# Kernel optimization log

Measured on AMD Instinct MI355X. Metric: run time of the kernel, lower is better.

The kernel has to match this reference:

```python
import jax, jax.numpy as jnp
import numpy as np

IN_F = 1024
OUT_F = 1024
GRID = 8
TOKENS = 8192


def setup_inputs() -> dict:
    key = jax.random.key(0)
    k_x, k_w, k_b, k_s = jax.random.split(key, 4)
    x = jax.random.normal(k_x, (TOKENS, IN_F), dtype=jnp.float32)
    # kaiming_uniform_(nonlinearity='linear'): bound = sqrt(3/fan_in)
    bound_w = float(np.sqrt(3.0 / IN_F))
    W = jax.random.uniform(k_w, (OUT_F, IN_F), minval=-bound_w, maxval=bound_w, dtype=jnp.float32)
    # nn.Linear default bias init: U(-1/sqrt(fan_in), 1/sqrt(fan_in))
    bound_b = float(1.0 / np.sqrt(IN_F))
    b = jax.random.uniform(k_b, (OUT_F,), minval=-bound_b, maxval=bound_b, dtype=jnp.float32)
    spline_weight = jax.random.uniform(k_s, (OUT_F, IN_F, GRID), minval=-0.1, maxval=0.1, dtype=jnp.float32)
    grid = jnp.linspace(-3.0, 3.0, GRID, dtype=jnp.float32)
    return {"x": x, "W": W, "b": b, "spline_weight": spline_weight, "grid": grid}


def reference(x, W, b, spline_weight, grid):
    grid_size = spline_weight.shape[-1]
    # base path: Linear(silu(x))
    base = jnp.einsum('ti,oi->to', jax.nn.silu(x), W) + b
    # RBF basis: [tokens, in_features, grid_size]
    denom = 2.0 / (grid_size - 1) + 1e-05
    basis = jnp.exp(-(((x[..., None] - grid) / denom) ** 2))
    spline = jnp.einsum('tig,oig->to', basis, spline_weight)
    return base + spline
```

## Files before the change

### kernel.cpp

```cpp
#include <hip/hip_runtime.h>
#include <hip/hip_bf16.h>

#define IN_F   1024
#define OUT_F  1024
#define GRID_N 8
#define TOKENS 8192
#define KTOT   9216
#define KHALF  4608
#define NTILE  72

typedef __attribute__((ext_vector_type(8))) short  bf16x8;
typedef __attribute__((ext_vector_type(4))) float  f32x4;

template<int M> struct ModeT { static constexpr int value = M; };

__device__ __forceinline__ unsigned int f2bf(float f) {
    union { float f; unsigned int u; } v; v.f = f;
    unsigned int r = v.u + 0x7fffu + ((v.u >> 16) & 1u);
    return r >> 16;
}

__global__ __launch_bounds__(256)
void prep_a_kernel(const float* __restrict__ x, const float* __restrict__ grid,
                   unsigned short* __restrict__ A)
{
    int idx = blockIdx.x * blockDim.x + threadIdx.x;
    int t = idx >> 10;
    int i = idx & 1023;
    float xv = x[idx];
    float sil = xv / (1.0f + __expf(-xv));
    A[(size_t)t * KTOT + i] = (unsigned short)f2bf(sil);

    const float invd = 1.0f / (2.0f / 7.0f + 1e-5f);
    unsigned int h[8];
    #pragma unroll
    for (int g = 0; g < 8; ++g) {
        float d = (xv - grid[g]) * invd;
        h[g] = f2bf(__expf(-d * d));
    }
    uint4 pk;
    pk.x = h[0] | (h[1] << 16);
    pk.y = h[2] | (h[3] << 16);
    pk.z = h[4] | (h[5] << 16);
    pk.w = h[6] | (h[7] << 16);
    *reinterpret_cast<uint4*>(&A[(size_t)t * KTOT + IN_F + (size_t)i * 8]) = pk;
}

__global__ __launch_bounds__(256)
void prep_b_kernel(const float* __restrict__ W, const float* __restrict__ spl,
                   unsigned short* __restrict__ B)
{
    int idx = blockIdx.x * blockDim.x + threadIdx.x;
    int o  = idx / (KTOT / 8);
    int c8 = idx - o * (KTOT / 8);
    const float* src = (c8 < IN_F / 8)
        ? (W   + (size_t)o * IN_F            + (size_t)c8 * 8)
        : (spl + (size_t)o * (IN_F * GRID_N) + (size_t)(c8 - IN_F / 8) * 8);
    const float4* s4 = reinterpret_cast<const float4*>(src);
    float4 lo = s4[0], hi = s4[1];
    uint4 pk;
    pk.x = f2bf(lo.x) | (f2bf(lo.y) << 16);
    pk.y = f2bf(lo.z) | (f2bf(lo.w) << 16);
    pk.z = f2bf(hi.x) | (f2bf(hi.y) << 16);
    pk.w = f2bf(hi.z) | (f2bf(hi.w) << 16);
    *reinterpret_cast<uint4*>(&B[(size_t)o * KTOT + (size_t)c8 * 8]) = pk;
}

#define GLOAD(src, dst) __builtin_amdgcn_global_load_lds( \
    (const __attribute__((address_space(1))) void*)(src),  \
    (__attribute__((address_space(3))) void*)(dst), 16, 0, 0)
#define SBAR()  __builtin_amdgcn_s_barrier()
#define SCH0()  __builtin_amdgcn_sched_barrier(0)
#define LGKM0() asm volatile("s_waitcnt lgkmcnt(0)" ::: "memory")
#define VMCNT_(n) asm volatile("s_waitcnt vmcnt(" #n ")" ::: "memory")

__global__ __launch_bounds__(512, 2)
void gemm_kan2(const unsigned short* __restrict__ A,
               const unsigned short* __restrict__ B,
               float* __restrict__ P, int rows)
{
    __shared__ char lds[131072];

    const int bid  = blockIdx.x;
    const int sk   = bid & 1;
    const int bn   = (bid >> 1) & 3;
    const int bm   = bid >> 3;
    const int tid  = threadIdx.x;
    const int wave = tid >> 6, lane = tid & 63;
    const int wr   = wave >> 2, wc = wave & 3;
    const int fr   = lane & 15, kg = lane >> 4;
    const int sw   = fr & 7;
    const int koff[2] = { (kg ^ sw) * 16, ((4 | kg) ^ sw) * 16 };
    const int k0 = sk * KHALF;

    const int trow = tid >> 3;
    const int ksrc = ((tid & 7) ^ (trow & 7)) * 8;
    const unsigned short* gA = A + (size_t)(bm * 256 + trow) * KTOT + k0 + ksrc;
    const unsigned short* gB = B + (size_t)(bn * 256 + trow) * KTOT + k0 + ksrc;
    const size_t R64 = (size_t)64 * KTOT;

    f32x4 acc[8][4];
    const f32x4 zero = {0.f, 0.f, 0.f, 0.f};
    #pragma unroll
    for (int m = 0; m < 8; ++m)
        #pragma unroll
        for (int n = 0; n < 4; ++n) acc[m][n] = zero;

    {
        char* d = lds + tid * 16;
        GLOAD(gA,           d);            GLOAD(gA + R64,     d + 8192);
        GLOAD(gB,           d + 32768);    GLOAD(gB + R64,     d + 40960);
        GLOAD(gB + 2 * R64, d + 49152);    GLOAD(gB + 3 * R64, d + 57344);
        GLOAD(gA + 2 * R64, d + 16384);    GLOAD(gA + 3 * R64, d + 24576);
        gA += 64; gB += 64;
        d += 65536;
        GLOAD(gA,           d);            GLOAD(gA + R64,     d + 8192);
        GLOAD(gB,           d + 32768);    GLOAD(gB + R64,     d + 40960);
        GLOAD(gB + 2 * R64, d + 49152);    GLOAD(gB + 3 * R64, d + 57344);
        GLOAD(gA + 2 * R64, d + 16384);    GLOAD(gA + 3 * R64, d + 24576);
        gA += 64; gB += 64;
    }
    VMCNT_(12); SBAR(); SCH0();

    const int aOff = (wr * 64 + fr) * 128;
    const int bOff = 32768 + (wc * 32 + fr) * 128;

    bf16x8 af[4][2], bfLo[2][2], bfHi[2][2];
    int u = 0;

    auto tile = [&](auto mC) {
        constexpr int MODE = decltype(mC)::value;
        char* bufc = lds + (u & 1) * 65536;
        char* d    = bufc + tid * 16;

        #pragma unroll
        for (int mi = 0; mi < 4; ++mi)
            #pragma unroll
            for (int ks = 0; ks < 2; ++ks)
                af[mi][ks] = *(const bf16x8*)(bufc + aOff + mi * 2048 + koff[ks]);
        #pragma unroll
        for (int ni = 0; ni < 2; ++ni)
            #pragma unroll
            for (int ks = 0; ks < 2; ++ks)
                bfLo[ni][ks] = *(const bf16x8*)(bufc + bOff + ni * 2048 + koff[ks]);
        if constexpr (MODE == 0) { VMCNT_(10); }
        else if constexpr (MODE == 1) { VMCNT_(10); }
        else { VMCNT_(2); }
        SBAR(); SCH0(); LGKM0(); SCH0();
        __builtin_amdgcn_s_setprio(1);
        #pragma unroll
        for (int mi = 0; mi < 4; ++mi)
            #pragma unroll
            for (int ni = 0; ni < 2; ++ni)
                #pragma unroll
                for (int ks = 0; ks < 2; ++ks)
                    acc[mi][ni] = __builtin_amdgcn_mfma_f32_16x16x32_bf16(
                        af[mi][ks], bfLo[ni][ks], acc[mi][ni], 0, 0, 0);
        __builtin_amdgcn_s_setprio(0);
        SBAR(); SCH0();

        #pragma unroll
        for (int ni = 0; ni < 2; ++ni)
            #pragma unroll
            for (int ks = 0; ks < 2; ++ks)
                bfHi[ni][ks] = *(const bf16x8*)(bufc + bOff + 16384 + ni * 2048 + koff[ks]);
        if constexpr (MODE == 0) {
            GLOAD(gA,       d);            GLOAD(gA + R64, d + 8192);
            GLOAD(gB,       d + 32768);    GLOAD(gB + R64, d + 40960);
            VMCNT_(12);
        } else if constexpr (MODE == 1) { VMCNT_(8); }
        else { VMCNT_(0); }
        SBAR(); SCH0(); LGKM0(); SCH0();
        __builtin_amdgcn_s_setprio(1);
        #pragma unroll
        for (int mi = 0; mi < 4; ++mi)
            #pragma unroll
            for (int ni = 0; ni < 2; ++ni)
                #pragma unroll
                for (int ks = 0; ks < 2; ++ks)
                    acc[mi][2 + ni] = __builtin_amdgcn_mfma_f32_16x16x32_bf16(
                        af[mi][ks], bfHi[ni][ks], acc[mi][2 + ni], 0, 0, 0);
        __builtin_amdgcn_s_setprio(0);
        SBAR(); SCH0();

        #pragma unroll
        for (int mi = 0; mi < 4; ++mi)
            #pragma unroll
            for (int ks = 0; ks < 2; ++ks)
                af[mi][ks] = *(const bf16x8*)(bufc + aOff + 16384 + mi * 2048 + koff[ks]);
        if constexpr (MODE == 0) {
            GLOAD(gB + 2 * R64, d + 49152);  GLOAD(gB + 3 * R64, d + 57344);
        }
        SBAR(); SCH0(); LGKM0(); SCH0();
        __builtin_amdgcn_s_setprio(1);
        #pragma unroll
        for (int mi = 0; mi < 4; ++mi)
            #pragma unroll
            for (int ni = 0; ni < 2; ++ni)
                #pragma unroll
                for (int ks = 0; ks < 2; ++ks)
                    acc[4 + mi][2 + ni] = __builtin_amdgcn_mfma_f32_16x16x32_bf16(
                        af[mi][ks], bfHi[ni][ks], acc[4 + mi][2 + ni], 0, 0, 0);
        __builtin_amdgcn_s_setprio(0);
        SBAR(); SCH0();

        if constexpr (MODE == 0) {
            GLOAD(gA + 2 * R64, d + 16384);  GLOAD(gA + 3 * R64, d + 24576);
            VMCNT_(12);
        } else if constexpr (MODE == 1) { VMCNT_(4); }
        SBAR(); SCH0();
        __builtin_amdgcn_s_setprio(1);
        #pragma unroll
        for (int mi = 0; mi < 4; ++mi)
            #pragma unroll
            for (int ni = 0; ni < 2; ++ni)
                #pragma unroll
                for (int ks = 0; ks < 2; ++ks)
                    acc[4 + mi][ni] = __builtin_amdgcn_mfma_f32_16x16x32_bf16(
                        af[mi][ks], bfLo[ni][ks], acc[4 + mi][ni], 0, 0, 0);
        __builtin_amdgcn_s_setprio(0);
        SBAR(); SCH0();

        if constexpr (MODE == 0) { gA += 64; gB += 64; }
    };

    for (u = 0; u < NTILE - 2; ++u) tile(ModeT<0>{});
    tile(ModeT<1>{});
    ++u;
    tile(ModeT<2>{});

    float* Pp = P + (size_t)sk * rows * OUT_F;
    const size_t orow0 = (size_t)bm * 256 + (size_t)wr * 64;
    const int    ocol0 = bn * 256 + wc * 32;
    #pragma unroll
    for (int n = 0; n < 4; ++n) {
        const int col = ocol0 + (n & 1) * 16 + (n >> 1) * 128 + fr;
        #pragma unroll
        for (int m = 0; m < 8; ++m) {
            const size_t r0 = orow0 + (m & 3) * 16 + (m >> 2) * 128 + kg * 4;
            #pragma unroll
            for (int j = 0; j < 4; ++j)
                Pp[(r0 + j) * OUT_F + col] = acc[m][n][j];
        }
    }
}

__global__ __launch_bounds__(256)
void reduce_kan(const float* __restrict__ P, const float* __restrict__ bias,
                float* __restrict__ out, int n4, int skStride4)
{
    const float4* p0 = (const float4*)P;
    const float4* p1 = p0 + skStride4;
    const float4* bv = (const float4*)bias;
    float4* o = (float4*)out;
    for (int i = blockIdx.x * blockDim.x + threadIdx.x; i < n4;
         i += gridDim.x * blockDim.x) {
        float4 a = p0[i], b = p1[i], c = bv[i & 255];
        float4 r;
        r.x = a.x + b.x + c.x;  r.y = a.y + b.y + c.y;
        r.z = a.z + b.z + c.z;  r.w = a.w + b.w + c.w;
        o[i] = r;
    }
}

extern "C" void kernel_launch(void* const* d_in, const int* in_sizes, int n_in,
                              void* d_out, int out_size, void* d_ws, size_t ws_size,
                              hipStream_t stream)
{
    const float* x    = (const float*)d_in[0];
    const float* W    = (const float*)d_in[1];
    const float* bias = (const float*)d_in[2];
    const float* spl  = (const float*)d_in[3];
    const float* grid = (const float*)d_in[4];
    float* out = (float*)d_out;

    unsigned short* Bw = (unsigned short*)d_ws;
    unsigned short* Aw = Bw + (size_t)OUT_F * KTOT;

    const size_t bBytes = (size_t)OUT_F * KTOT * 2;
    size_t avail = ws_size > bBytes ? ws_size - bBytes : 0;
    long maxRows = (long)(avail / 26624);
    int chunk = (maxRows >= TOKENS) ? TOKENS : (int)((maxRows / 256) * 256);
    if (chunk < 256) chunk = 256;
    float* Pp = (float*)(Aw + (size_t)chunk * KTOT);

    prep_b_kernel<<<(OUT_F * (KTOT / 8)) / 256, 256, 0, stream>>>(W, spl, Bw);

    for (int t0 = 0; t0 < TOKENS; t0 += chunk) {
        int rows = (TOKENS - t0 < chunk) ? (TOKENS - t0) : chunk;
        prep_a_kernel<<<(rows * IN_F) / 256, 256, 0, stream>>>(
            x + (size_t)t0 * IN_F, grid, Aw);
        gemm_kan2<<<(rows >> 8) * 8, 512, 0, stream>>>(Aw, Bw, Pp, rows);
        int n4 = rows * 256;
        int rblocks = (n4 + 255) / 256; if (rblocks > 2048) rblocks = 2048;
        reduce_kan<<<rblocks, 256, 0, stream>>>(
            Pp, bias, out + (size_t)t0 * OUT_F, n4, n4);
    }
}
```

Before: 202.4 us.

## Replace staggered multi-barrier GEMM pipeline with simple per-tile double buffering

Reorganizes LDS into separate A and B double buffers. All eight global-to-LDS loads for the next K tile are now issued at the start of each tile, and the kernel waits with a single vmcnt(0) and one barrier at the end. The previous interleaved schedule used partial vmcnt waits and barriers between each MFMA cluster; this removes those barriers to cut synchronisation cost. In exchange it loses the fine-grained overlap of loads with compute, and it exposes a full memory wait at every tile boundary.

New measurement: 195.2 us. 3.6% less time.

```diff
diff --git a/kernel.cpp b/kernel.cpp
--- a/kernel.cpp
+++ b/kernel.cpp
@@ -3,7 +3,6 @@
 
 #define IN_F   1024
 #define OUT_F  1024
-#define GRID_N 8
 #define TOKENS 8192
 #define KTOT   9216
 #define KHALF  4608
@@ -54,8 +53,8 @@
     int o  = idx / (KTOT / 8);
     int c8 = idx - o * (KTOT / 8);
     const float* src = (c8 < IN_F / 8)
-        ? (W   + (size_t)o * IN_F            + (size_t)c8 * 8)
-        : (spl + (size_t)o * (IN_F * GRID_N) + (size_t)(c8 - IN_F / 8) * 8);
+        ? (W   + (size_t)o * IN_F     + (size_t)c8 * 8)
+        : (spl + (size_t)o * IN_F * 8 + (size_t)(c8 - IN_F / 8) * 8);
     const float4* s4 = reinterpret_cast<const float4*>(src);
     float4 lo = s4[0], hi = s4[1];
     uint4 pk;
@@ -71,8 +70,7 @@
     (__attribute__((address_space(3))) void*)(dst), 16, 0, 0)
 #define SBAR()  __builtin_amdgcn_s_barrier()
 #define SCH0()  __builtin_amdgcn_sched_barrier(0)
-#define LGKM0() asm volatile("s_waitcnt lgkmcnt(0)" ::: "memory")
-#define VMCNT_(n) asm volatile("s_waitcnt vmcnt(" #n ")" ::: "memory")
+#define VMC0()  asm volatile("s_waitcnt vmcnt(0)" ::: "memory")
 
 __global__ __launch_bounds__(512, 2)
 void gemm_kan2(const unsigned short* __restrict__ A,
@@ -107,46 +105,51 @@
         for (int n = 0; n < 4; ++n) acc[m][n] = zero;
 
     {
-        char* d = lds + tid * 16;
-        GLOAD(gA,           d);            GLOAD(gA + R64,     d + 8192);
-        GLOAD(gB,           d + 32768);    GLOAD(gB + R64,     d + 40960);
-        GLOAD(gB + 2 * R64, d + 49152);    GLOAD(gB + 3 * R64, d + 57344);
-        GLOAD(gA + 2 * R64, d + 16384);    GLOAD(gA + 3 * R64, d + 24576);
+        char* dA = lds + tid * 16;
+        char* dB = lds + 65536 + tid * 16;
+        GLOAD(gA,           dA);           GLOAD(gA + R64,     dA + 8192);
+        GLOAD(gA + 2 * R64, dA + 16384);   GLOAD(gA + 3 * R64, dA + 24576);
+        GLOAD(gB,           dB);           GLOAD(gB + R64,     dB + 8192);
+        GLOAD(gB + 2 * R64, dB + 16384);   GLOAD(gB + 3 * R64, dB + 24576);
         gA += 64; gB += 64;
-        d += 65536;
-        GLOAD(gA,           d);            GLOAD(gA + R64,     d + 8192);
-        GLOAD(gB,           d + 32768);    GLOAD(gB + R64,     d + 40960);
-        GLOAD(gB + 2 * R64, d + 49152);    GLOAD(gB + 3 * R64, d + 57344);
-        GLOAD(gA + 2 * R64, d + 16384);    GLOAD(gA + 3 * R64, d + 24576);
-        gA += 64; gB += 64;
-    }
-    VMCNT_(12); SBAR(); SCH0();
+    }
+    VMC0(); SBAR(); SCH0();
 
     const int aOff = (wr * 64 + fr) * 128;
-    const int bOff = 32768 + (wc * 32 + fr) * 128;
+    const int bOff = (wc * 32 + fr) * 128;
 
     bf16x8 af[4][2], bfLo[2][2], bfHi[2][2];
     int u = 0;
 
     auto tile = [&](auto mC) {
         constexpr int MODE = decltype(mC)::value;
-        char* bufc = lds + (u & 1) * 65536;
-        char* d    = bufc + tid * 16;
+        char* bufA = lds + (u & 1) * 32768;
+        char* bufB = lds + 65536 + (u & 1) * 32768;
 
         #pragma unroll
         for (int mi = 0; mi < 4; ++mi)
             #pragma unroll
             for (int ks = 0; ks < 2; ++ks)
-                af[mi][ks] = *(const bf16x8*)(bufc + aOff + mi * 2048 + koff[ks]);
+                af[mi][ks] = *(const bf16x8*)(bufA + aOff + mi * 2048 + koff[ks]);
         #pragma unroll
         for (int ni = 0; ni < 2; ++ni)
             #pragma unroll
-            for (int ks = 0; ks < 2; ++ks)
-                bfLo[ni][ks] = *(const bf16x8*)(bufc + bOff + ni * 2048 + koff[ks]);
-        if constexpr (MODE == 0) { VMCNT_(10); }
-        else if constexpr (MODE == 1) { VMCNT_(10); }
-        else { VMCNT_(2); }
-        SBAR(); SCH0(); LGKM0(); SCH0();
+            for (int ks = 0; ks < 2; ++ks) {
+                bfLo[ni][ks] = *(const bf16x8*)(bufB + bOff + ni * 2048 + koff[ks]);
+                bfHi[ni][ks] = *(const bf16x8*)(bufB + bOff + 16384 + ni * 2048 + koff[ks]);
+            }
+
+        if constexpr (MODE == 0) {
+            char* dA = lds + ((u & 1) ^ 1) * 32768 + tid * 16;
+            char* dB = lds + 65536 + ((u & 1) ^ 1) * 32768 + tid * 16;
+            GLOAD(gA,           dA);           GLOAD(gA + R64,     dA + 8192);
+            GLOAD(gA + 2 * R64, dA + 16384);   GLOAD(gA + 3 * R64, dA + 24576);
+            GLOAD(gB,           dB);           GLOAD(gB + R64,     dB + 8192);
+            GLOAD(gB + 2 * R64, dB + 16384);   GLOAD(gB + 3 * R64, dB + 24576);
+            gA += 64; gB += 64;
+        }
+        SCH0();
+
         __builtin_amdgcn_s_setprio(1);
         #pragma unroll
         for (int mi = 0; mi < 4; ++mi)
@@ -157,20 +160,7 @@
                     acc[mi][ni] = __builtin_amdgcn_mfma_f32_16x16x32_bf16(
                         af[mi][ks], bfLo[ni][ks], acc[mi][ni], 0, 0, 0);
         __builtin_amdgcn_s_setprio(0);
-        SBAR(); SCH0();
-
-        #pragma unroll
-        for (int ni = 0; ni < 2; ++ni)
-            #pragma unroll
-            for (int ks = 0; ks < 2; ++ks)
-                bfHi[ni][ks] = *(const bf16x8*)(bufc + bOff + 16384 + ni * 2048 + koff[ks]);
-        if constexpr (MODE == 0) {
-            GLOAD(gA,       d);            GLOAD(gA + R64, d + 8192);
-            GLOAD(gB,       d + 32768);    GLOAD(gB + R64, d + 40960);
-            VMCNT_(12);
-        } else if constexpr (MODE == 1) { VMCNT_(8); }
-        else { VMCNT_(0); }
-        SBAR(); SCH0(); LGKM0(); SCH0();
+
         __builtin_amdgcn_s_setprio(1);
         #pragma unroll
         for (int mi = 0; mi < 4; ++mi)
@@ -181,17 +171,24 @@
                     acc[mi][2 + ni] = __builtin_amdgcn_mfma_f32_16x16x32_bf16(
                         af[mi][ks], bfHi[ni][ks], acc[mi][2 + ni], 0, 0, 0);
         __builtin_amdgcn_s_setprio(0);
-        SBAR(); SCH0();
 
         #pragma unroll
         for (int mi = 0; mi < 4; ++mi)
             #pragma unroll
             for (int ks = 0; ks < 2; ++ks)
-                af[mi][ks] = *(const bf16x8*)(bufc + aOff + 16384 + mi * 2048 + koff[ks]);
-        if constexpr (MODE == 0) {
-            GLOAD(gB + 2 * R64, d + 49152);  GLOAD(gB + 3 * R64, d + 57344);
-        }
-        SBAR(); SCH0(); LGKM0(); SCH0();
+                af[mi][ks] = *(const bf16x8*)(bufA + aOff + 16384 + mi * 2048 + koff[ks]);
+
+        __builtin_amdgcn_s_setprio(1);
+        #pragma unroll
+        for (int mi = 0; mi < 4; ++mi)
+            #pragma unroll
+            for (int ni = 0; ni < 2; ++ni)
+                #pragma unroll
+                for (int ks = 0; ks < 2; ++ks)
+                    acc[4 + mi][ni] = __builtin_amdgcn_mfma_f32_16x16x32_bf16(
+                        af[mi][ks], bfLo[ni][ks], acc[4 + mi][ni], 0, 0, 0);
+        __builtin_amdgcn_s_setprio(0);
+
         __builtin_amdgcn_s_setprio(1);
         #pragma unroll
         for (int mi = 0; mi < 4; ++mi)
@@ -202,32 +199,16 @@
                     acc[4 + mi][2 + ni] = __builtin_amdgcn_mfma_f32_16x16x32_bf16(
                         af[mi][ks], bfHi[ni][ks], acc[4 + mi][2 + ni], 0, 0, 0);
         __builtin_amdgcn_s_setprio(0);
-        SBAR(); SCH0();
-
+
+        SCH0();
         if constexpr (MODE == 0) {
-            GLOAD(gA + 2 * R64, d + 16384);  GLOAD(gA + 3 * R64, d + 24576);
-            VMCNT_(12);
-        } else if constexpr (MODE == 1) { VMCNT_(4); }
-        SBAR(); SCH0();
-        __builtin_amdgcn_s_setprio(1);
-        #pragma unroll
-        for (int mi = 0; mi < 4; ++mi)
-            #pragma unroll
-            for (int ni = 0; ni < 2; ++ni)
-                #pragma unroll
-                for (int ks = 0; ks < 2; ++ks)
-                    acc[4 + mi][ni] = __builtin_amdgcn_mfma_f32_16x16x32_bf16(
-                        af[mi][ks], bfLo[ni][ks], acc[4 + mi][ni], 0, 0, 0);
-        __builtin_amdgcn_s_setprio(0);
-        SBAR(); SCH0();
-
-        if constexpr (MODE == 0) { gA += 64; gB += 64; }
+            VMC0();
+            SBAR(); SCH0();
+        }
     };
 
-    for (u = 0; u < NTILE - 2; ++u) tile(ModeT<0>{});
+    for (u = 0; u < NTILE - 1; ++u) tile(ModeT<0>{});
     tile(ModeT<1>{});
-    ++u;
-    tile(ModeT<2>{});
 
     float* Pp = P + (size_t)sk * rows * OUT_F;
     const size_t orow0 = (size_t)bm * 256 + (size_t)wr * 64;
```
